# Performance work log

Hardware: AMD Instinct MI355X
Metric: run time of the kernel (lower is better)

The kernel has to match this reference:

```python
import jax, jax.numpy as jnp
import numpy as np

B, D, NA, RANK, H = 8192, 64, 64, 32, 16  # B = n_envs * NA, n_envs = 128


def setup_inputs() -> dict:
    key = jax.random.key(0)
    k = jax.random.split(key, 6)
    x = jax.random.normal(k[0], (B, D, NA), dtype=jnp.float32)
    L = jax.random.randint(k[1], (B, 1, NA), 0, 2).astype(jnp.float32)
    Aq = jax.random.normal(k[2], (RANK, D), dtype=jnp.float32)
    Ak = jax.random.normal(k[3], (RANK, D), dtype=jnp.float32)
    Av = jax.random.normal(k[4], (RANK, D), dtype=jnp.float32)
    Ao = jax.random.normal(k[5], (H, RANK), dtype=jnp.float32)
    return {"x": x, "L": L, "Aq": Aq, "Ak": Ak, "Av": Av, "Ao": Ao}


def reference(x, L, Aq, Ak, Av, Ao):
    b, d, na = x.shape
    E = b // na  # number of environments
    h = Ao.shape[0]  # must be 16 (stride-16 block assembly)

    # numNeighbors per batch element: count of L[:,0,:] >= 1, plus self
    numN = jnp.sum((L[:, 0, :] >= 1.0).astype(x.dtype), axis=1)[:, None, None] + 1.0

    # low-rank attention: Q,K,V are [B, r, na]
    Q = jnp.tanh(jnp.einsum('rd,bdn->brn', Aq, x))
    K = jnp.tanh(jnp.einsum('rd,bdn->brn', Ak, x))
    V = jnp.tanh(jnp.einsum('rd,bdn->brn', Av, x))
    scores = jnp.einsum('brn,bsn->brs', Q, K) / jnp.sqrt(numN)  # [B, r, r]
    attn = jax.nn.softmax(scores, axis=2)
    o = jnp.einsum('brs,bsn->brn', attn, V)  # [B, r, na]

    Rh = jnp.tanh(jnp.einsum('hr,brn->bhn', Ao, o))  # [B, h, na]
    R = (Rh.reshape(E, na, h * na)) ** 2  # [E, na, 16*na]

    # The 16 strided scatters Rupper[:, rows, cols] = R[:, :, k::16] are
    # equivalent to a reshape+transpose: channel c = j*16 + k with
    # k = 8*hr + 4*hc + 2*pr + pc, row = hr*2na + 2i + pr, col = hc*2na + 2j + pc.
    T = R.reshape(E, na, na, 2, 2, 2, 2)         # [E, i, j, hr, hc, pr, pc]
    T = jnp.transpose(T, (0, 3, 1, 5, 4, 2, 6))  # [E, hr, i, pr, hc, j, pc]
    Rupper = T.reshape(E, 4 * na, 4 * na)

    # symmetrize
    Rupper = Rupper + jnp.transpose(Rupper, (0, 2, 1))

    n4 = 4 * na
    eye = jnp.eye(n4, dtype=x.dtype)
    diag = jnp.diagonal(Rupper, axis1=1, axis2=2)  # [E, 4na]
    Rdiag = Rupper * (1.0 - eye)                   # off-diagonal part
    rowsum = jnp.sum(Rdiag, axis=2)                # [E, 4na]
    # diagonal = diag(Rupper) + rowsum(offdiag); offdiag = -Rdiag
    Rout = eye * (diag + rowsum)[:, :, None] - Rdiag
    return Rout
```

## Files before the change

### kernel.cpp

```cpp
#include <hip/hip_runtime.h>
#include <math.h>

#define Bn 8192
#define Ee 128
#define EB 4

typedef __attribute__((ext_vector_type(8))) short short8;
typedef __attribute__((ext_vector_type(4))) float f32x4;

__device__ __forceinline__ float fast_tanh(float x) {
    float e = __expf(2.f * x);
    return fmaf(-2.f, __builtin_amdgcn_rcpf(1.f + e), 1.f);
}

__device__ __forceinline__ unsigned int bf1(float a) {
    return (__builtin_bit_cast(unsigned int, a) + 0x8000u) >> 16;
}
__device__ __forceinline__ unsigned int pack2bf(float a, float b) {
    unsigned int ua = (__builtin_bit_cast(unsigned int, a) + 0x8000u) >> 16;
    unsigned int ub = (__builtin_bit_cast(unsigned int, b) + 0x8000u) & 0xffff0000u;
    return ua | ub;
}

__global__ __launch_bounds__(256)
void att_prep(const float* __restrict__ Aq, const float* __restrict__ Ak,
              const float* __restrict__ Av, const float* __restrict__ Ao,
              short* __restrict__ Abf) {
    const int t = threadIdx.x;
    const float* Am[3] = {Aq, Ak, Av};
#pragma unroll
    for (int mat = 0; mat < 3; ++mat) {
        float4 v0 = *(const float4*)(Am[mat] + t * 8);
        float4 v1 = *(const float4*)(Am[mat] + t * 8 + 4);
        uint4 pk = {pack2bf(v0.x, v0.y), pack2bf(v0.z, v0.w),
                    pack2bf(v1.x, v1.y), pack2bf(v1.z, v1.w)};
        *(uint4*)&Abf[mat * 2048 + t * 8] = pk;
    }
    if (t < 64) {
        float4 v0 = *(const float4*)(Ao + t * 8);
        float4 v1 = *(const float4*)(Ao + t * 8 + 4);
        uint4 pk = {pack2bf(v0.x, v0.y), pack2bf(v0.z, v0.w),
                    pack2bf(v1.x, v1.y), pack2bf(v1.z, v1.w)};
        *(uint4*)&Abf[6144 + t * 8] = pk;
    }
}

__global__ __launch_bounds__(256, 2)
void att_m2(const float* __restrict__ x, const float* __restrict__ L,
            const short* __restrict__ Abf, float* __restrict__ R) {
    const int b0   = blockIdx.x * EB;
    const int t    = threadIdx.x;
    const int lane = t & 63;
    const int w    = t >> 6;
    const int q    = lane >> 4;
    const int m    = lane & 15;

    __shared__ __align__(16) short sQot[EB][2560];
    __shared__ __align__(16) short sK[EB][2304];
    __shared__ __align__(16) short sVt[EB][2560];
    __shared__ __align__(16) short sP[EB][1280];
    __shared__ float sNum[EB];

    float xf[EB][16];
#pragma unroll
    for (int e = 0; e < EB; ++e) {
        const float* p0 = x + (size_t)(b0 + e) * 4096 + (q * 8) * 64 + (w * 16 + m);
#pragma unroll
        for (int j = 0; j < 8; ++j) xf[e][j] = p0[j * 64];
        const float* p1 = p0 + 32 * 64;
#pragma unroll
        for (int j = 0; j < 8; ++j) xf[e][8 + j] = p1[j * 64];
    }

    short8 bfr[3][2][2];
#pragma unroll
    for (int mat = 0; mat < 3; ++mat)
#pragma unroll
        for (int rt = 0; rt < 2; ++rt) {
            const short* Ab = Abf + mat * 2048 + (rt * 16 + m) * 64 + q * 8;
            bfr[mat][rt][0] = *(const short8*)Ab;
            bfr[mat][rt][1] = *(const short8*)(Ab + 32);
        }
    short8 aa = *(const short8*)&Abf[6144 + m * 32 + q * 8];

    {
        const int e = w;
        float lv = L[(size_t)(b0 + e) * 64 + lane];
        unsigned long long mk = __ballot(lv >= 1.0f);
        if (lane == 0) sNum[e] = (float)__popcll(mk) + 1.0f;
    }

    short8 afr[EB][2];
#pragma unroll
    for (int e = 0; e < EB; ++e) {
        uint4 pk0 = {pack2bf(xf[e][0], xf[e][1]), pack2bf(xf[e][2], xf[e][3]),
                     pack2bf(xf[e][4], xf[e][5]), pack2bf(xf[e][6], xf[e][7])};
        uint4 pk1 = {pack2bf(xf[e][8], xf[e][9]), pack2bf(xf[e][10], xf[e][11]),
                     pack2bf(xf[e][12], xf[e][13]), pack2bf(xf[e][14], xf[e][15])};
        afr[e][0] = __builtin_bit_cast(short8, pk0);
        afr[e][1] = __builtin_bit_cast(short8, pk1);
    }
#pragma unroll
    for (int mat = 0; mat < 3; ++mat) {
#pragma unroll
        for (int rt = 0; rt < 2; ++rt) {
#pragma unroll
            for (int e = 0; e < EB; ++e) {
                f32x4 c = {0.f, 0.f, 0.f, 0.f};
                c = __builtin_amdgcn_mfma_f32_16x16x32_bf16(afr[e][0], bfr[mat][rt][0], c, 0, 0, 0);
                c = __builtin_amdgcn_mfma_f32_16x16x32_bf16(afr[e][1], bfr[mat][rt][1], c, 0, 0, 0);
                float tv[4];
#pragma unroll
                for (int j = 0; j < 4; ++j) tv[j] = fast_tanh(c[j]);
                if (mat < 2) {
                    uint2 p2 = {pack2bf(tv[0], tv[1]), pack2bf(tv[2], tv[3])};
                    short* dst = (mat == 0) ? sQot[e] : sK[e];
                    *(uint2*)&dst[(rt * 16 + m) * 72 + (w * 16 + q * 4)] = p2;
                } else {
#pragma unroll
                    for (int j = 0; j < 4; ++j)
                        sVt[e][(w * 16 + q * 4 + j) * 40 + (rt * 16 + m)] = (short)bf1(tv[j]);
                }
            }
        }
    }
    __syncthreads();

    const int wr = w & 1, ws = w >> 1;
#pragma unroll
    for (int e = 0; e < EB; ++e) {
        short8 qa0 = *(const short8*)&sQot[e][(wr * 16 + m) * 72 + q * 8];
        short8 qa1 = *(const short8*)&sQot[e][(wr * 16 + m) * 72 + 32 + q * 8];
        short8 kb0 = *(const short8*)&sK[e][(ws * 16 + m) * 72 + q * 8];
        short8 kb1 = *(const short8*)&sK[e][(ws * 16 + m) * 72 + 32 + q * 8];
        f32x4 c = {0.f, 0.f, 0.f, 0.f};
        c = __builtin_amdgcn_mfma_f32_16x16x32_bf16(qa0, kb0, c, 0, 0, 0);
        c = __builtin_amdgcn_mfma_f32_16x16x32_bf16(qa1, kb1, c, 0, 0, 0);
        float inv = rsqrtf(sNum[e]);
#pragma unroll
        for (int j = 0; j < 4; ++j) {
            float p = __expf(c[j] * inv);
            sP[e][(wr * 16 + q * 4 + j) * 40 + ws * 16 + m] = (short)bf1(p);
        }
    }
    __syncthreads();

    {
        short8 ones;
#pragma unroll
        for (int j = 0; j < 8; ++j) ones[j] = (short)0x3F80;
#pragma unroll
        for (int e = 0; e < EB; ++e) {
            short* ot = sQot[e];
            short8 vb = *(const short8*)&sVt[e][(w * 16 + m) * 40 + q * 8];
#pragma unroll
            for (int rt = 0; rt < 2; ++rt) {
                short8 pa = *(const short8*)&sP[e][(rt * 16 + m) * 40 + q * 8];
                f32x4 z = {0.f, 0.f, 0.f, 0.f};
                f32x4 crs = __builtin_amdgcn_mfma_f32_16x16x32_bf16(pa, ones, z, 0, 0, 0);
                f32x4 cpv = __builtin_amdgcn_mfma_f32_16x16x32_bf16(pa, vb, z, 0, 0, 0);
                float ov[4];
#pragma unroll
                for (int j = 0; j < 4; ++j)
                    ov[j] = cpv[j] * __builtin_amdgcn_rcpf(crs[j]);
                uint2 p2 = {pack2bf(ov[0], ov[1]), pack2bf(ov[2], ov[3])};
                *(uint2*)&ot[(w * 16 + m) * 40 + (rt * 16 + q * 4)] = p2;
            }
        }
    }

#pragma unroll
    for (int e = 0; e < EB; ++e) {
        const short* ot = sQot[e];
        short8 bb = *(const short8*)&ot[(w * 16 + m) * 40 + q * 8];
        f32x4 c = {0.f, 0.f, 0.f, 0.f};
        c = __builtin_amdgcn_mfma_f32_16x16x32_bf16(aa, bb, c, 0, 0, 0);
        float* Rb = R + (size_t)(b0 + e) * 1024;
#pragma unroll
        for (int j = 0; j < 4; ++j) {
            float rh = fast_tanh(c[j]);
            Rb[(q * 4 + j) * 64 + w * 16 + m] = rh * rh;
        }
    }
}

__global__ __launch_bounds__(256)
void att_k2(const float* __restrict__ R, float* __restrict__ out) {
    const int e   = blockIdx.x >> 6;
    const int rg  = blockIdx.x & 63;
    const int w   = threadIdx.x >> 6;
    const int j   = threadIdx.x & 63;
    const int row = rg * 4 + w;
    const int hr = row >> 7, i = (row >> 1) & 63, pr = row & 1;

    const float* Re = R + (size_t)e * 65536;
    float* Oe       = out + (size_t)e * 65536;

    const float* t1p = Re + i * 1024 + j * 16 + 8 * hr + 2 * pr;
    float2 t1a = *(const float2*)t1p;
    float2 t1b = *(const float2*)(t1p + 4);
    const float* t2p = Re + j * 1024 + i * 16 + 4 * hr + pr;
    float c00 = t1a.x + t2p[0];
    float c01 = t1a.y + t2p[2];
    float c10 = t1b.x + t2p[8];
    float c11 = t1b.y + t2p[10];

    float sum = c00 + c01 + c10 + c11;
#pragma unroll
    for (int off = 32; off >= 1; off >>= 1) sum += __shfl_xor(sum, off);

    float v00 = -c00, v01 = -c01, v10 = -c10, v11 = -c11;
    if (j == i) {
        if (hr == 0) { if (pr == 0) v00 = sum; else v01 = sum; }
        else         { if (pr == 0) v10 = sum; else v11 = sum; }
    }
    float2 z0 = {v00, v01}, z1 = {v10, v11};
    *(float2*)&Oe[row * 256 + 2 * j]       = z0;
    *(float2*)&Oe[row * 256 + 128 + 2 * j] = z1;
}

__global__ __launch_bounds__(256, 4)
void att_k1_atomic(const float* __restrict__ x, const float* __restrict__ L,
                   const float* __restrict__ Aq, const float* __restrict__ Ak,
                   const float* __restrict__ Av, const float* __restrict__ Ao,
                   float* __restrict__ out) {
    const int b    = blockIdx.x;
    const int t    = threadIdx.x;
    const int lane = t & 63;
    const int w    = t >> 6;
    const int wu   = __builtin_amdgcn_readfirstlane(w);

    __shared__ float sQ[32][68];
    __shared__ float sK[32][68];
    __shared__ float sV[32][68];
    __shared__ float sNum;

    const float* xb = x + (size_t)b * 4096;
    if (t < 64) {
        float lv = L[(size_t)b * 64 + t];
        unsigned long long mk = __ballot(lv >= 1.0f);
        if (t == 0) sNum = (float)__popcll(mk) + 1.0f;
    }
    float acc[3][8];
#pragma unroll
    for (int mm = 0; mm < 3; ++mm)
#pragma unroll
        for (int k = 0; k < 8; ++k) acc[mm][k] = 0.f;
    const float* Am[3] = {Aq, Ak, Av};
#pragma unroll
    for (int hf = 0; hf < 2; ++hf) {
        float xv[32];
#pragma unroll
        for (int d = 0; d < 32; ++d) xv[d] = xb[(hf * 32 + d) * 64 + lane];
#pragma unroll
        for (int mm = 0; mm < 3; ++mm)
#pragma unroll
            for (int k = 0; k < 8; ++k) {
                const float* Ar = Am[mm] + (wu + 4 * k) * 64 + hf * 32;
                float a = acc[mm][k];
#pragma unroll
                for (int d = 0; d < 32; ++d) a = fmaf(Ar[d], xv[d], a);
                acc[mm][k] = a;
            }
    }
    float(*const sMat[3])[68] = {sQ, sK, sV};
#pragma unroll
    for (int mm = 0; mm < 3; ++mm)
#pragma unroll
        for (int k = 0; k < 8; ++k)
            sMat[mm][wu + 4 * k][lane] = fast_tanh(acc[mm][k]);
    __syncthreads();

    const int s = lane & 31, half = lane >> 5;
    const float inv = rsqrtf(sNum);
    float kreg[32];
#pragma unroll
    for (int c = 0; c < 8; ++c) {
        float4 kv = *(const float4*)&sK[s][half * 32 + 4 * c];
        kreg[4 * c] = kv.x; kreg[4 * c + 1] = kv.y;
        kreg[4 * c + 2] = kv.z; kreg[4 * c + 3] = kv.w;
    }
    float sc8[8];
#pragma unroll
    for (int kk = 0; kk < 8; ++kk) {
        float sc = 0.f;
#pragma unroll
        for (int c = 0; c < 8; ++c) {
            float4 qv = *(const float4*)&sQ[wu + 4 * kk][half * 32 + 4 * c];
            sc = fmaf(qv.x, kreg[4 * c], sc);
            sc = fmaf(qv.y, kreg[4 * c + 1], sc);
            sc = fmaf(qv.z, kreg[4 * c + 2], sc);
            sc = fmaf(qv.w, kreg[4 * c + 3], sc);
        }
        sc += __shfl_xor(sc, 32);
        sc8[kk] = sc * inv;
    }
    float pown[4];
#pragma unroll
    for (int qq = 0; qq < 4; ++qq) pown[qq] = half ? sc8[2 * qq + 1] : sc8[2 * qq];
#pragma unroll
    for (int qq = 0; qq < 4; ++qq) {
        float e = __expf(pown[qq]);
        float ds = e;
#pragma unroll
        for (int off = 16; off >= 1; off >>= 1) ds += __shfl_xor(ds, off);
        pown[qq] = e * __builtin_amdgcn_rcpf(ds);
    }
    __syncthreads();
#pragma unroll
    for (int qq = 0; qq < 4; ++qq) sQ[wu + 8 * qq + 4 * half][s] = pown[qq];
    __syncthreads();
    float oacc[8];
#pragma unroll
    for (int k = 0; k < 8; ++k) oacc[k] = 0.f;
#pragma unroll
    for (int sb = 0; sb < 8; ++sb) {
        float4 arow[8];
#pragma unroll
        for (int kk = 0; kk < 8; ++kk) arow[kk] = *(const float4*)&sQ[wu + 4 * kk][4 * sb];
#pragma unroll
        for (int ds2 = 0; ds2 < 4; ++ds2) {
            float vv = sV[4 * sb + ds2][lane];
#pragma unroll
            for (int kk = 0; kk < 8; ++kk) {
                float a = (ds2 == 0) ? arow[kk].x : (ds2 == 1) ? arow[kk].y
                        : (ds2 == 2) ? arow[kk].z : arow[kk].w;
                oacc[kk] = fmaf(a, vv, oacc[kk]);
            }
        }
    }
#pragma unroll
    for (int k = 0; k < 8; ++k) sK[wu + 4 * k][lane] = oacc[k];
    __syncthreads();
    float col[32];
#pragma unroll
    for (int r = 0; r < 32; ++r) col[r] = sK[r][lane];
#pragma unroll
    for (int k = 0; k < 4; ++k) {
        const int h = wu + 4 * k;
        const float* AoR = Ao + h * 32;
        float a2 = 0.f;
#pragma unroll
        for (int r = 0; r < 32; ++r) a2 = fmaf(AoR[r], col[r], a2);
        float rh = fast_tanh(a2);
        float val = rh * rh;
        const int e = b >> 6, i = b & 63;
        const int c = h * 64 + lane;
        const int jj = c >> 4, k4 = c & 15;
        const int hr = (k4 >> 3) & 1, hc = (k4 >> 2) & 1;
        const int pr = (k4 >> 1) & 1, pc = k4 & 1;
        const int row = hr * 128 + 2 * i + pr;
        const int colo = hc * 128 + 2 * jj + pc;
        float* oe = out + (size_t)e * 65536;
        atomicAdd(&oe[row * 256 + colo], val);
        atomicAdd(&oe[colo * 256 + row], val);
    }
}

__global__ __launch_bounds__(256)
void att_k3(float* __restrict__ out) {
    const size_t rowbase = (size_t)blockIdx.x * 256;
    const int t = threadIdx.x;
    float v = out[rowbase + t];
    float sum = v;
#pragma unroll
    for (int off = 32; off >= 1; off >>= 1) sum += __shfl_xor(sum, off);
    __shared__ float red[4];
    if ((t & 63) == 0) red[t >> 6] = sum;
    __syncthreads();
    float tot = red[0] + red[1] + red[2] + red[3];
    const int row = blockIdx.x & 255;
    out[rowbase + t] = (t == row) ? tot : -v;
}

extern "C" void kernel_launch(void* const* d_in, const int* in_sizes, int n_in,
                              void* d_out, int out_size, void* d_ws, size_t ws_size,
                              hipStream_t stream) {
    const float* x  = (const float*)d_in[0];
    const float* L  = (const float*)d_in[1];
    const float* Aq = (const float*)d_in[2];
    const float* Ak = (const float*)d_in[3];
    const float* Av = (const float*)d_in[4];
    const float* Ao = (const float*)d_in[5];
    float* out = (float*)d_out;

    const size_t rbytes = (size_t)Bn * 1024 * sizeof(float);
    const size_t need   = rbytes + 6656 * sizeof(short);
    if (ws_size >= need) {
        float* R   = (float*)d_ws;
        short* Abf = (short*)((char*)d_ws + rbytes);
        att_prep<<<1, 256, 0, stream>>>(Aq, Ak, Av, Ao, Abf);
        att_m2<<<Bn / EB, 256, 0, stream>>>(x, L, Abf, R);
        att_k2<<<Ee * 64, 256, 0, stream>>>(R, out);
    } else {
        (void)hipMemsetAsync(d_out, 0, (size_t)out_size * sizeof(float), stream);
        att_k1_atomic<<<Bn, 256, 0, stream>>>(x, L, Aq, Ak, Av, Ao, out);
        att_k3<<<Ee * 256, 256, 0, stream>>>(out);
    }
}
```

Measured before the change: 75.89 us.

## Store intermediate R as bf16 and halve per-block batch for higher occupancy

The intermediate R buffer written by the attention kernel and read by the assembly kernel is now stored as bf16 instead of fp32. This halves workspace traffic between the two kernels. Separately, each block now handles 2 batch elements instead of 4, and launch bounds target 4 blocks per SM to raise occupancy. The change adds bf16 rounding error on R before symmetrization and summation, which could affect accuracy, and it reduces per-block work amortization.

```diff
diff --git a/kernel.cpp b/kernel.cpp
--- a/kernel.cpp
+++ b/kernel.cpp
@@ -3,7 +3,7 @@
 
 #define Bn 8192
 #define Ee 128
-#define EB 4
+#define EB 2
 
 typedef __attribute__((ext_vector_type(8))) short short8;
 typedef __attribute__((ext_vector_type(4))) float f32x4;
@@ -20,6 +20,9 @@
     unsigned int ua = (__builtin_bit_cast(unsigned int, a) + 0x8000u) >> 16;
     unsigned int ub = (__builtin_bit_cast(unsigned int, b) + 0x8000u) & 0xffff0000u;
     return ua | ub;
+}
+__device__ __forceinline__ float bf2f(unsigned int u) {
+    return __builtin_bit_cast(float, u << 16);
 }
 
 __global__ __launch_bounds__(256)
@@ -45,9 +48,9 @@
     }
 }
 
-__global__ __launch_bounds__(256, 2)
+__global__ __launch_bounds__(256, 4)
 void att_m2(const float* __restrict__ x, const float* __restrict__ L,
-            const short* __restrict__ Abf, float* __restrict__ R) {
+            const short* __restrict__ Abf, unsigned short* __restrict__ R) {
     const int b0   = blockIdx.x * EB;
     const int t    = threadIdx.x;
     const int lane = t & 63;
@@ -83,11 +86,11 @@
         }
     short8 aa = *(const short8*)&Abf[6144 + m * 32 + q * 8];
 
-    {
-        const int e = w;
-        float lv = L[(size_t)(b0 + e) * 64 + lane];
+    if (t < 64 * EB) {
+        const int e = t >> 6;
+        float lv = L[(size_t)(b0 + e) * 64 + (t & 63)];
         unsigned long long mk = __ballot(lv >= 1.0f);
-        if (lane == 0) sNum[e] = (float)__popcll(mk) + 1.0f;
+        if ((t & 63) == 0) sNum[e] = (float)__popcll(mk) + 1.0f;
     }
 
     short8 afr[EB][2];
@@ -175,17 +178,17 @@
         short8 bb = *(const short8*)&ot[(w * 16 + m) * 40 + q * 8];
         f32x4 c = {0.f, 0.f, 0.f, 0.f};
         c = __builtin_amdgcn_mfma_f32_16x16x32_bf16(aa, bb, c, 0, 0, 0);
-        float* Rb = R + (size_t)(b0 + e) * 1024;
+        unsigned short* Rb = R + (size_t)(b0 + e) * 1024;
 #pragma unroll
         for (int j = 0; j < 4; ++j) {
             float rh = fast_tanh(c[j]);
-            Rb[(q * 4 + j) * 64 + w * 16 + m] = rh * rh;
+            Rb[(q * 4 + j) * 64 + w * 16 + m] = (unsigned short)bf1(rh * rh);
         }
     }
 }
 
 __global__ __launch_bounds__(256)
-void att_k2(const float* __restrict__ R, float* __restrict__ out) {
+void att_k2(const unsigned short* __restrict__ R, float* __restrict__ out) {
     const int e   = blockIdx.x >> 6;
     const int rg  = blockIdx.x & 63;
     const int w   = threadIdx.x >> 6;
@@ -193,17 +196,17 @@
     const int row = rg * 4 + w;
     const int hr = row >> 7, i = (row >> 1) & 63, pr = row & 1;
 
-    const float* Re = R + (size_t)e * 65536;
-    float* Oe       = out + (size_t)e * 65536;
-
-    const float* t1p = Re + i * 1024 + j * 16 + 8 * hr + 2 * pr;
-    float2 t1a = *(const float2*)t1p;
-    float2 t1b = *(const float2*)(t1p + 4);
-    const float* t2p = Re + j * 1024 + i * 16 + 4 * hr + pr;
-    float c00 = t1a.x + t2p[0];
-    float c01 = t1a.y + t2p[2];
-    float c10 = t1b.x + t2p[8];
-    float c11 = t1b.y + t2p[10];
+    const unsigned short* Re = R + (size_t)e * 65536;
+    float* Oe = out + (size_t)e * 65536;
+
+    const unsigned short* t1p = Re + i * 1024 + j * 16 + 8 * hr + 2 * pr;
+    unsigned int a0 = *(const unsigned int*)t1p;
+    unsigned int a1 = *(const unsigned int*)(t1p + 4);
+    const unsigned short* t2p = Re + j * 1024 + i * 16 + 4 * hr + pr;
+    float c00 = bf2f(a0 & 0xffffu)  + bf2f(t2p[0]);
+    float c01 = bf2f(a0 >> 16)      + bf2f(t2p[2]);
+    float c10 = bf2f(a1 & 0xffffu)  + bf2f(t2p[8]);
+    float c11 = bf2f(a1 >> 16)      + bf2f(t2p[10]);
 
     float sum = c00 + c01 + c10 + c11;
 #pragma unroll
@@ -384,10 +387,10 @@
     const float* Ao = (const float*)d_in[5];
     float* out = (float*)d_out;
 
-    const size_t rbytes = (size_t)Bn * 1024 * sizeof(float);
+    const size_t rbytes = (size_t)Bn * 1024 * sizeof(unsigned short);
     const size_t need   = rbytes + 6656 * sizeof(short);
     if (ws_size >= need) {
-        float* R   = (float*)d_ws;
+        unsigned short* R = (unsigned short*)d_ws;
         short* Abf = (short*)((char*)d_ws + rbytes);
         att_prep<<<1, 256, 0, stream>>>(Aq, Ak, Av, Ao, Abf);
         att_m2<<<Bn / EB, 256, 0, stream>>>(x, L, Abf, R);
```

Measured after the change: 74.03 us. 2.5% less time.

## Drop weight-prep kernel, convert weights in-kernel, halve batch per block

Applied to the files above, without the earlier changes.

Removes the separate att_prep launch that converted the projection weights to bf16. Each att_m2 block now loads the fp32 weights and packs them to bf16 fragments itself. EB drops from 4 to 2, which doubles the grid and raises the launch-bounds occupancy hint from 2 to 4 blocks per CU. The intent is to cut one kernel launch and its serialization and to improve latency hiding. In exchange, every block repeats the weight conversion and reads twice as many bytes of weights.

```diff
diff --git a/kernel.cpp b/kernel.cpp
--- a/kernel.cpp
+++ b/kernel.cpp
@@ -3,7 +3,7 @@
 
 #define Bn 8192
 #define Ee 128
-#define EB 4
+#define EB 2
 
 typedef __attribute__((ext_vector_type(8))) short short8;
 typedef __attribute__((ext_vector_type(4))) float f32x4;
@@ -21,33 +21,17 @@
     unsigned int ub = (__builtin_bit_cast(unsigned int, b) + 0x8000u) & 0xffff0000u;
     return ua | ub;
 }
-
-__global__ __launch_bounds__(256)
-void att_prep(const float* __restrict__ Aq, const float* __restrict__ Ak,
-              const float* __restrict__ Av, const float* __restrict__ Ao,
-              short* __restrict__ Abf) {
-    const int t = threadIdx.x;
-    const float* Am[3] = {Aq, Ak, Av};
-#pragma unroll
-    for (int mat = 0; mat < 3; ++mat) {
-        float4 v0 = *(const float4*)(Am[mat] + t * 8);
-        float4 v1 = *(const float4*)(Am[mat] + t * 8 + 4);
-        uint4 pk = {pack2bf(v0.x, v0.y), pack2bf(v0.z, v0.w),
-                    pack2bf(v1.x, v1.y), pack2bf(v1.z, v1.w)};
-        *(uint4*)&Abf[mat * 2048 + t * 8] = pk;
-    }
-    if (t < 64) {
-        float4 v0 = *(const float4*)(Ao + t * 8);
-        float4 v1 = *(const float4*)(Ao + t * 8 + 4);
-        uint4 pk = {pack2bf(v0.x, v0.y), pack2bf(v0.z, v0.w),
-                    pack2bf(v1.x, v1.y), pack2bf(v1.z, v1.w)};
-        *(uint4*)&Abf[6144 + t * 8] = pk;
-    }
-}
-
-__global__ __launch_bounds__(256, 2)
+__device__ __forceinline__ short8 packfrag(float4 v0, float4 v1) {
+    uint4 pk = {pack2bf(v0.x, v0.y), pack2bf(v0.z, v0.w),
+                pack2bf(v1.x, v1.y), pack2bf(v1.z, v1.w)};
+    return __builtin_bit_cast(short8, pk);
+}
+
+__global__ __launch_bounds__(256, 4)
 void att_m2(const float* __restrict__ x, const float* __restrict__ L,
-            const short* __restrict__ Abf, float* __restrict__ R) {
+            const float* __restrict__ Aq, const float* __restrict__ Ak,
+            const float* __restrict__ Av, const float* __restrict__ Ao,
+            float* __restrict__ R) {
     const int b0   = blockIdx.x * EB;
     const int t    = threadIdx.x;
     const int lane = t & 63;
@@ -73,21 +57,28 @@
     }
 
     short8 bfr[3][2][2];
-#pragma unroll
-    for (int mat = 0; mat < 3; ++mat)
-#pragma unroll
-        for (int rt = 0; rt < 2; ++rt) {
-            const short* Ab = Abf + mat * 2048 + (rt * 16 + m) * 64 + q * 8;
-            bfr[mat][rt][0] = *(const short8*)Ab;
-            bfr[mat][rt][1] = *(const short8*)(Ab + 32);
-        }
-    short8 aa = *(const short8*)&Abf[6144 + m * 32 + q * 8];
-
     {
-        const int e = w;
-        float lv = L[(size_t)(b0 + e) * 64 + lane];
+        const float* Am[3] = {Aq, Ak, Av};
+#pragma unroll
+        for (int mat = 0; mat < 3; ++mat)
+#pragma unroll
+            for (int rt = 0; rt < 2; ++rt) {
+                const float* Ab = Am[mat] + (rt * 16 + m) * 64 + q * 8;
+                bfr[mat][rt][0] = packfrag(*(const float4*)Ab, *(const float4*)(Ab + 4));
+                bfr[mat][rt][1] = packfrag(*(const float4*)(Ab + 32), *(const float4*)(Ab + 36));
+            }
+    }
+    short8 aa;
+    {
+        const float* Aob = Ao + m * 32 + q * 8;
+        aa = packfrag(*(const float4*)Aob, *(const float4*)(Aob + 4));
+    }
+
+    if (t < 64 * EB) {
+        const int e = t >> 6;
+        float lv = L[(size_t)(b0 + e) * 64 + (t & 63)];
         unsigned long long mk = __ballot(lv >= 1.0f);
-        if (lane == 0) sNum[e] = (float)__popcll(mk) + 1.0f;
+        if ((t & 63) == 0) sNum[e] = (float)__popcll(mk) + 1.0f;
     }
 
     short8 afr[EB][2];
@@ -384,13 +375,10 @@
     const float* Ao = (const float*)d_in[5];
     float* out = (float*)d_out;
 
-    const size_t rbytes = (size_t)Bn * 1024 * sizeof(float);
-    const size_t need   = rbytes + 6656 * sizeof(short);
+    const size_t need = (size_t)Bn * 1024 * sizeof(float);
     if (ws_size >= need) {
-        float* R   = (float*)d_ws;
-        short* Abf = (short*)((char*)d_ws + rbytes);
-        att_prep<<<1, 256, 0, stream>>>(Aq, Ak, Av, Ao, Abf);
-        att_m2<<<Bn / EB, 256, 0, stream>>>(x, L, Abf, R);
+        float* R = (float*)d_ws;
+        att_m2<<<Bn / EB, 256, 0, stream>>>(x, L, Aq, Ak, Av, Ao, R);
         att_k2<<<Ee * 64, 256, 0, stream>>>(R, out);
     } else {
         (void)hipMemsetAsync(d_out, 0, (size_t)out_size * sizeof(float), stream);
```

Measured after the change: 152.6 us. 101% more time.
